# Kernel tuning notes

Measured on AMD Instinct MI355X. Metric: run time of the kernel, lower is better.

## Reference

```python
import jax, jax.numpy as jnp
import numpy as np

BN_EPS = 1e-5
HIDDEN = 64
NUM_LAYERS = 8


def setup_inputs() -> dict:
    key = jax.random.key(0)
    ks = jax.random.split(key, 24)
    N, E, G = 100000, 1600000, 500
    H, L = HIDDEN, NUM_LAYERS
    rn = lambda k, s, sc=0.1: jax.random.normal(k, s, jnp.float32) * sc
    un = lambda k, s: jax.random.uniform(k, s, jnp.float32, 0.5, 1.5)
    inp = {}
    inp["x"] = jax.random.normal(ks[0], (N, 1), jnp.float32)
    inp["edge_index"] = jax.random.randint(ks[1], (2, E), 0, N, jnp.int32)
    inp["batch"] = jnp.sort(jax.random.randint(ks[2], (N,), 0, G, jnp.int32))
    inp["num_graphs"] = G
    inp["eps"] = rn(ks[3], (L,))
    inp["W1_first"] = rn(ks[4], (1, H))
    inp["W1_rest"] = rn(ks[5], (L - 1, H, H))
    inp["b1"] = rn(ks[6], (L, H))
    inp["g1"] = un(ks[7], (L, H))
    inp["be1"] = rn(ks[8], (L, H))
    inp["m1"] = rn(ks[9], (L, H))
    inp["v1"] = un(ks[10], (L, H))
    inp["W2"] = rn(ks[11], (L, H, H))
    inp["b2"] = rn(ks[12], (L, H))
    inp["g2"] = un(ks[13], (L, H))
    inp["be2"] = rn(ks[14], (L, H))
    inp["m2"] = rn(ks[15], (L, H))
    inp["v2"] = un(ks[16], (L, H))
    inp["lin1_w"] = rn(ks[17], (L * H, H), 0.05)
    inp["lin1_b"] = rn(ks[18], (H,))
    inp["lin2_w"] = rn(ks[19], (H, 3))
    inp["lin2_b"] = rn(ks[20], (3,))
    return inp


def _bn(h, g, b, m, v):
    # BatchNorm1d in eval mode: affine normalize with running stats
    return (h - m) * jax.lax.rsqrt(v + BN_EPS) * g + b


def reference(x, edge_index, batch, num_graphs, eps, W1_first, W1_rest, b1, g1,
              be1, m1, v1, W2, b2, g2, be2, m2, v2, lin1_w, lin1_b, lin2_w, lin2_b):
    src, dst = edge_index[0], edge_index[1]
    N = x.shape[0]
    h = x
    xs = []
    for i in range(NUM_LAYERS):
        # GINConv: scatter-add neighbor aggregation + (1+eps)*self, then MLP
        agg = jax.ops.segment_sum(h[src], dst, num_segments=N)  # [N, H_in]
        z = (1.0 + eps[i]) * h + agg
        W1 = W1_first if i == 0 else W1_rest[i - 1]
        z = jnp.maximum(z @ W1 + b1[i], 0.0)
        z = _bn(z, g1[i], be1[i], m1[i], v1[i])
        z = jnp.maximum(z @ W2[i] + b2[i], 0.0)
        z = _bn(z, g2[i], be2[i], m2[i], v2[i])
        h = z
        xs.append(h)
    jk = jnp.concatenate(xs, axis=-1)  # [N, L*H] JumpingKnowledge 'cat'
    sums = jax.ops.segment_sum(jk, batch, num_segments=num_graphs)
    counts = jax.ops.segment_sum(jnp.ones((N,), jk.dtype), batch, num_segments=num_graphs)
    pooled = sums / jnp.maximum(counts, 1.0)[:, None]  # global_mean_pool
    h = jnp.maximum(pooled @ lin1_w + lin1_b, 0.0)
    # dropout is identity in eval mode
    logits = h @ lin2_w + lin2_b
    return jax.nn.log_softmax(logits, axis=-1)
```

## Files before the change

kernel.cpp:

```cpp
#include <hip/hip_runtime.h>
#include <hip/hip_bf16.h>
#include <math.h>


typedef unsigned int uint;
typedef unsigned short ushort;
typedef __attribute__((ext_vector_type(8))) short short8;
typedef __attribute__((ext_vector_type(4))) float floatx4;
typedef __attribute__((ext_vector_type(4))) uint uintx4;

#define BBITS 10
#define BCAP 20480
#define BMASK ((1 << BBITS) - 1)

__device__ __forceinline__ float bf_lo(uint w) { return __uint_as_float(w << 16); }
__device__ __forceinline__ float bf_hi(uint w) { return __uint_as_float(w & 0xffff0000u); }

__device__ __forceinline__ ushort f2bf(float x) {
  __hip_bfloat16 h = __float2bfloat16(x);
  return *(ushort*)&h;
}
__device__ __forceinline__ float bf2f(ushort u) { return __uint_as_float((uint)u << 16); }

__device__ __forceinline__ uint pack_bf16(float a, float b) {
  return (uint)f2bf(a) | ((uint)f2bf(b) << 16);
}

__device__ __forceinline__ float slot_combine(float v) {
  return v + __shfl_xor(v, 8, 64);
}

__device__ __forceinline__ void split8(float4 u0, float4 u1, short8& hi, short8& lo) {
  float v0 = u0.x, v1 = u0.y, v2 = u0.z, v3 = u0.w;
  float v4 = u1.x, v5 = u1.y, v6 = u1.z, v7 = u1.w;
  ushort h0 = f2bf(v0), h1 = f2bf(v1), h2 = f2bf(v2), h3 = f2bf(v3);
  ushort h4 = f2bf(v4), h5 = f2bf(v5), h6 = f2bf(v6), h7 = f2bf(v7);
  hi[0] = (short)h0; hi[1] = (short)h1; hi[2] = (short)h2; hi[3] = (short)h3;
  hi[4] = (short)h4; hi[5] = (short)h5; hi[6] = (short)h6; hi[7] = (short)h7;
  lo[0] = (short)f2bf(v0 - bf2f(h0)); lo[1] = (short)f2bf(v1 - bf2f(h1));
  lo[2] = (short)f2bf(v2 - bf2f(h2)); lo[3] = (short)f2bf(v3 - bf2f(h3));
  lo[4] = (short)f2bf(v4 - bf2f(h4)); lo[5] = (short)f2bf(v5 - bf2f(h5));
  lo[6] = (short)f2bf(v6 - bf2f(h6)); lo[7] = (short)f2bf(v7 - bf2f(h7));
}


__global__ void init_bc_kernel(int* __restrict__ bc, int NB) {
  int b = threadIdx.x;
  if (b < NB) bc[b * 16] = b * BCAP;
}

__global__ __launch_bounds__(1024) void bin_edges_kernel(
    const int* __restrict__ src, const int* __restrict__ dst, int* __restrict__ bc,
    uint* __restrict__ arena, int E) {
  __shared__ int cnt[128], base[128];
  for (long chunk = (long)blockIdx.x * 4096; chunk < E; chunk += (long)gridDim.x * 4096) {
    if (threadIdx.x < 128) cnt[threadIdx.x] = 0;
    __syncthreads();
    uint v[4];
    int b[4], r[4];
#pragma unroll
    for (int u = 0; u < 4; ++u) {
      long e = chunk + threadIdx.x + u * 1024;
      if (e < E) {
        int s = src[e];
        int d = dst[e];
        b[u] = d >> BBITS;
        v[u] = ((uint)s << BBITS) | (uint)(d & BMASK);
        r[u] = atomicAdd(&cnt[b[u]], 1);
      }
    }
    __syncthreads();
    if (threadIdx.x < 128)
      base[threadIdx.x] = cnt[threadIdx.x] ? atomicAdd(&bc[threadIdx.x * 16], cnt[threadIdx.x]) : 0;
    __syncthreads();
#pragma unroll
    for (int u = 0; u < 4; ++u) {
      long e = chunk + threadIdx.x + u * 1024;
      if (e < E) arena[base[b[u]] + r[u]] = v[u];
    }
    __syncthreads();
  }
}

__global__ __launch_bounds__(1024) void bucket_count_kernel(
    const uint* __restrict__ arena, const int* __restrict__ bc,
    int* __restrict__ deg, int N) {
  __shared__ int hist[1 << BBITS];
  int b = blockIdx.x;
  int lo = b << BBITS;
  int hi = min(lo + (1 << BBITS), N);
  hist[threadIdx.x] = 0;
  __syncthreads();
  int cnt = bc[b * 16] - b * BCAP;
  const uint* ad = arena + (size_t)b * BCAP;
  for (int i = threadIdx.x; i < cnt; i += 1024) atomicAdd(&hist[ad[i] & BMASK], 1);
  __syncthreads();
  if (lo + (int)threadIdx.x < hi) deg[lo + threadIdx.x] = hist[threadIdx.x];
}

__global__ __launch_bounds__(1024) void bucket_scatter_kernel(
    const uint* __restrict__ arena, const int* __restrict__ bc,
    const int* __restrict__ rp, int* __restrict__ col, int N) {
  __shared__ int cur[1 << BBITS];
  int b = blockIdx.x;
  int lo = b << BBITS;
  int hi = min(lo + (1 << BBITS), N);
  if (lo + (int)threadIdx.x < hi) cur[threadIdx.x] = rp[lo + threadIdx.x];
  __syncthreads();
  int cnt = bc[b * 16] - b * BCAP;
  const uint* ad = arena + (size_t)b * BCAP;
  for (int i = threadIdx.x; i < cnt; i += 1024) {
    uint v = ad[i];
    int pos = atomicAdd(&cur[v & BMASK], 1);
    col[pos] = (int)(v >> BBITS);
  }
}

__global__ void scan_blocksums(const int* __restrict__ deg, int* __restrict__ bsum, int N) {
  __shared__ int red[256];
  int i = blockIdx.x * 256 + threadIdx.x;
  red[threadIdx.x] = (i < N) ? deg[i] : 0;
  __syncthreads();
  for (int off = 128; off > 0; off >>= 1) {
    if (threadIdx.x < off) red[threadIdx.x] += red[threadIdx.x + off];
    __syncthreads();
  }
  if (threadIdx.x == 0) bsum[blockIdx.x] = red[0];
}

__global__ void scan_bsum(const int* __restrict__ bsum, int* __restrict__ boff,
                          int* __restrict__ rp_last, int B) {
  __shared__ int tmp[1024];
  int t = threadIdx.x;
  int v = (t < B) ? bsum[t] : 0;
  tmp[t] = v;
  __syncthreads();
  for (int off = 1; off < 1024; off <<= 1) {
    int u = (t >= off) ? tmp[t - off] : 0;
    __syncthreads();
    tmp[t] += u;
    __syncthreads();
  }
  if (t < B) boff[t] = tmp[t] - v;
  if (t == 1023) *rp_last = tmp[1023];
}

__global__ void scan_final(const int* __restrict__ deg, const int* __restrict__ boff,
                           int* __restrict__ rp, int N) {
  __shared__ int tmp[256];
  int i = blockIdx.x * 256 + threadIdx.x;
  int v = (i < N) ? deg[i] : 0;
  tmp[threadIdx.x] = v;
  __syncthreads();
  for (int off = 1; off < 256; off <<= 1) {
    int u = (threadIdx.x >= off) ? tmp[threadIdx.x - off] : 0;
    __syncthreads();
    tmp[threadIdx.x] += u;
    __syncthreads();
  }
  if (i < N) rp[i] = boff[blockIdx.x] + tmp[threadIdx.x] - v;
}

__global__ void graph_bounds_kernel(const int* __restrict__ batch, int* __restrict__ gs,
                                    int N, int G) {
  int n = blockIdx.x * 256 + threadIdx.x;
  if (n >= N) return;
  int b = batch[n];
  int bp = (n == 0) ? -1 : batch[n - 1];
  for (int g = bp + 1; g <= b; ++g) gs[g] = n;
  if (n == N - 1)
    for (int g = b + 1; g <= G; ++g) gs[g] = N;
}

__global__ void prepack_w_kernel(const float* __restrict__ W1_rest,
                                 const float* __restrict__ W2, ushort* __restrict__ wp) {
  int l = blockIdx.x >> 1, g = blockIdx.x & 1;
  const float* W;
  if (g == 0) {
    if (l == 0) return;
    W = W1_rest + (size_t)(l - 1) * 4096;
  } else {
    W = W2 + (size_t)l * 4096;
  }
  ushort* out = wp + (size_t)(l * 2 + g) * 8192;
  for (int idx = threadIdx.x; idx < 4096; idx += blockDim.x) {
    int j = idx & 7, lane = (idx >> 3) & 63, ks = (idx >> 9) & 1, nt = (idx >> 10) & 3;
    int k = ks * 32 + (lane >> 4) * 8 + j;
    int n = nt * 16 + (lane & 15);
    float w = W[k * 64 + n];
    ushort hi = f2bf(w);
    ushort lo = f2bf(w - bf2f(hi));
    size_t base = (size_t)((nt * 2 + ks) * 2) * 512 + lane * 8 + j;
    out[base] = hi;
    out[base + 512] = lo;
  }
}

__global__ __launch_bounds__(256, 8) void agg_kernel(
    const ushort* __restrict__ hb, const int* __restrict__ rp,
    const int* __restrict__ col, const float* __restrict__ eps,
    int layer, ushort* __restrict__ zb, int N) {
  int lane = threadIdx.x & 63;
  int ni = lane >> 4;
  int s = (lane >> 3) & 1;
  int r = lane & 7;
  int wave = blockIdx.x * (blockDim.x >> 6) + (threadIdx.x >> 6);
  int nwaves = gridDim.x * (blockDim.x >> 6);
  float ep = 1.0f + eps[layer];
  for (int qb = wave * 4; qb < N; qb += nwaves * 4) {
    int node = qb + ni;
    bool valid = node < N;
    int nn = valid ? node : (N - 1);
    int beg = rp[nn];
    int end = valid ? rp[nn + 1] : beg;
    float a[8] = {0.f, 0.f, 0.f, 0.f, 0.f, 0.f, 0.f, 0.f};
    int e = beg + s;
    while (e < end) {
      int e1 = (e + 2 < end) ? (e + 2) : e;
      int e2 = (e + 4 < end) ? (e + 4) : e;
      int e3 = (e + 6 < end) ? (e + 6) : e;
      float m1 = (e + 2 < end) ? 1.0f : 0.0f;
      float m2 = (e + 4 < end) ? 1.0f : 0.0f;
      float m3 = (e + 6 < end) ? 1.0f : 0.0f;
      int c0 = __builtin_nontemporal_load(col + e);
      int c1 = __builtin_nontemporal_load(col + e1);
      int c2 = __builtin_nontemporal_load(col + e2);
      int c3 = __builtin_nontemporal_load(col + e3);
      uint4 w0 = ((const uint4*)(hb + (long)c0 * 64))[r];
      uint4 w1 = ((const uint4*)(hb + (long)c1 * 64))[r];
      uint4 w2 = ((const uint4*)(hb + (long)c2 * 64))[r];
      uint4 w3 = ((const uint4*)(hb + (long)c3 * 64))[r];
      a[0] += bf_lo(w0.x); a[1] += bf_hi(w0.x);
      a[2] += bf_lo(w0.y); a[3] += bf_hi(w0.y);
      a[4] += bf_lo(w0.z); a[5] += bf_hi(w0.z);
      a[6] += bf_lo(w0.w); a[7] += bf_hi(w0.w);
      a[0] = fmaf(m1, bf_lo(w1.x), a[0]); a[1] = fmaf(m1, bf_hi(w1.x), a[1]);
      a[2] = fmaf(m1, bf_lo(w1.y), a[2]); a[3] = fmaf(m1, bf_hi(w1.y), a[3]);
      a[4] = fmaf(m1, bf_lo(w1.z), a[4]); a[5] = fmaf(m1, bf_hi(w1.z), a[5]);
      a[6] = fmaf(m1, bf_lo(w1.w), a[6]); a[7] = fmaf(m1, bf_hi(w1.w), a[7]);
      a[0] = fmaf(m2, bf_lo(w2.x), a[0]); a[1] = fmaf(m2, bf_hi(w2.x), a[1]);
      a[2] = fmaf(m2, bf_lo(w2.y), a[2]); a[3] = fmaf(m2, bf_hi(w2.y), a[3]);
      a[4] = fmaf(m2, bf_lo(w2.z), a[4]); a[5] = fmaf(m2, bf_hi(w2.z), a[5]);
      a[6] = fmaf(m2, bf_lo(w2.w), a[6]); a[7] = fmaf(m2, bf_hi(w2.w), a[7]);
      a[0] = fmaf(m3, bf_lo(w3.x), a[0]); a[1] = fmaf(m3, bf_hi(w3.x), a[1]);
      a[2] = fmaf(m3, bf_lo(w3.y), a[2]); a[3] = fmaf(m3, bf_hi(w3.y), a[3]);
      a[4] = fmaf(m3, bf_lo(w3.z), a[4]); a[5] = fmaf(m3, bf_hi(w3.z), a[5]);
      a[6] = fmaf(m3, bf_lo(w3.w), a[6]); a[7] = fmaf(m3, bf_hi(w3.w), a[7]);
      e += 8;
    }
#pragma unroll
    for (int j = 0; j < 8; ++j) a[j] = slot_combine(a[j]);
    if (s == 0 && valid) {
      uint4 hv = ((const uint4*)(hb + (long)node * 64))[r];
      float v0 = fmaf(ep, bf_lo(hv.x), a[0]), v1 = fmaf(ep, bf_hi(hv.x), a[1]);
      float v2 = fmaf(ep, bf_lo(hv.y), a[2]), v3 = fmaf(ep, bf_hi(hv.y), a[3]);
      float v4 = fmaf(ep, bf_lo(hv.z), a[4]), v5 = fmaf(ep, bf_hi(hv.z), a[5]);
      float v6 = fmaf(ep, bf_lo(hv.w), a[6]), v7 = fmaf(ep, bf_hi(hv.w), a[7]);
      uintx4 w;
      w.x = pack_bf16(v0, v1); w.y = pack_bf16(v2, v3);
      w.z = pack_bf16(v4, v5); w.w = pack_bf16(v6, v7);
      __builtin_nontemporal_store(w, (uintx4*)(zb + (size_t)node * 64 + r * 8));
    }
  }
}

__global__ __launch_bounds__(512) void mfma_mlp_kernel(
    const ushort* __restrict__ zb, const float* __restrict__ z0,
    const float* __restrict__ W1f, ushort* __restrict__ hout,
    const ushort* __restrict__ wp1, const ushort* __restrict__ wp2,
    const float* __restrict__ b1, const float* __restrict__ g1,
    const float* __restrict__ be1, const float* __restrict__ m1,
    const float* __restrict__ v1,
    const float* __restrict__ b2, const float* __restrict__ g2,
    const float* __restrict__ be2, const float* __restrict__ m2,
    const float* __restrict__ v2,
    const int* __restrict__ batch, float* __restrict__ pooled,
    int layer, int skip1, int N) {
  __shared__ float bnp[6][64];
  __shared__ float w1fl[64];
  __shared__ float sbuf[128][68];
  __shared__ int batchl[128];
  int tid = threadIdx.x;
  int blockbase = blockIdx.x * 128;
  if (tid < 64) {
    bnp[0][tid] = b1[tid];
    float s1 = g1[tid] * rsqrtf(v1[tid] + 1e-5f);
    bnp[1][tid] = s1;
    bnp[2][tid] = be1[tid] - m1[tid] * s1;
    bnp[3][tid] = b2[tid];
    float s2 = g2[tid] * rsqrtf(v2[tid] + 1e-5f);
    bnp[4][tid] = s2;
    bnp[5][tid] = be2[tid] - m2[tid] * s2;
    if (skip1) w1fl[tid] = W1f[tid];
  }
  if (tid < 128) batchl[tid] = (blockbase + tid < N) ? batch[blockbase + tid] : -1;
  __syncthreads();
  int wave = tid >> 6, lane = tid & 63;
  int q = lane >> 4, c = lane & 15;
  int base = blockbase + wave * 16;
  int srow = wave * 16;

  short8 ahi0, alo0, ahi1, alo1;
  if (!skip1) {
    {
      long row = base + c;
      if (row >= N) row = N - 1;
      const ushort* zr = zb + row * 64;
      ahi0 = __builtin_nontemporal_load((const short8*)(zr + q * 8));
      ahi1 = __builtin_nontemporal_load((const short8*)(zr + 32 + q * 8));
    }
    floatx4 acc[4];
#pragma unroll
    for (int nt = 0; nt < 4; ++nt) acc[nt] = (floatx4){0.f, 0.f, 0.f, 0.f};
#pragma unroll
    for (int nt = 0; nt < 4; ++nt) {
#pragma unroll
      for (int ks = 0; ks < 2; ++ks) {
        const ushort* fb = wp1 + ((nt * 2 + ks) * 2) * 512 + lane * 8;
        short8 bh = *(const short8*)fb;
        short8 bl = *(const short8*)(fb + 512);
        short8 ah = ks ? ahi1 : ahi0;
        acc[nt] = __builtin_amdgcn_mfma_f32_16x16x32_bf16(ah, bh, acc[nt], 0, 0, 0);
        acc[nt] = __builtin_amdgcn_mfma_f32_16x16x32_bf16(ah, bl, acc[nt], 0, 0, 0);
      }
    }
#pragma unroll
    for (int nt = 0; nt < 4; ++nt) {
      int feat = nt * 16 + c;
      float s1 = bnp[1][feat], o1 = bnp[2][feat], bb = bnp[0][feat];
#pragma unroll
      for (int r = 0; r < 4; ++r) {
        float y = fmaxf(acc[nt][r] + bb, 0.f);
        sbuf[srow + q * 4 + r][feat] = fmaf(y, s1, o1);
      }
    }
    float4 u0 = *(const float4*)&sbuf[srow + c][q * 8];
    float4 u1 = *(const float4*)&sbuf[srow + c][q * 8 + 4];
    split8(u0, u1, ahi0, alo0);
    u0 = *(const float4*)&sbuf[srow + c][32 + q * 8];
    u1 = *(const float4*)&sbuf[srow + c][32 + q * 8 + 4];
    split8(u0, u1, ahi1, alo1);
  } else {
    long row = base + c;
    if (row >= N) row = N - 1;
    float zv = z0[row];
    float4 t00, t01, t10, t11;
    {
      float tv[8];
#pragma unroll
      for (int j = 0; j < 8; ++j) {
        int k = q * 8 + j;
        float y = fmaxf(fmaf(zv, w1fl[k], bnp[0][k]), 0.f);
        tv[j] = fmaf(y, bnp[1][k], bnp[2][k]);
      }
      t00 = make_float4(tv[0], tv[1], tv[2], tv[3]);
      t01 = make_float4(tv[4], tv[5], tv[6], tv[7]);
#pragma unroll
      for (int j = 0; j < 8; ++j) {
        int k = 32 + q * 8 + j;
        float y = fmaxf(fmaf(zv, w1fl[k], bnp[0][k]), 0.f);
        tv[j] = fmaf(y, bnp[1][k], bnp[2][k]);
      }
      t10 = make_float4(tv[0], tv[1], tv[2], tv[3]);
      t11 = make_float4(tv[4], tv[5], tv[6], tv[7]);
    }
    split8(t00, t01, ahi0, alo0);
    split8(t10, t11, ahi1, alo1);
  }

  floatx4 acc2[4];
#pragma unroll
  for (int nt = 0; nt < 4; ++nt) acc2[nt] = (floatx4){0.f, 0.f, 0.f, 0.f};
#pragma unroll
  for (int nt = 0; nt < 4; ++nt) {
#pragma unroll
    for (int ks = 0; ks < 2; ++ks) {
      const ushort* fb = wp2 + ((nt * 2 + ks) * 2) * 512 + lane * 8;
      short8 bh = *(const short8*)fb;
      short8 bl = *(const short8*)(fb + 512);
      short8 ah = ks ? ahi1 : ahi0;
      short8 al = ks ? alo1 : alo0;
      acc2[nt] = __builtin_amdgcn_mfma_f32_16x16x32_bf16(ah, bh, acc2[nt], 0, 0, 0);
      acc2[nt] = __builtin_amdgcn_mfma_f32_16x16x32_bf16(al, bh, acc2[nt], 0, 0, 0);
      acc2[nt] = __builtin_amdgcn_mfma_f32_16x16x32_bf16(ah, bl, acc2[nt], 0, 0, 0);
    }
  }

#pragma unroll
  for (int nt = 0; nt < 4; ++nt) {
    int feat = nt * 16 + c;
    float s2 = bnp[4][feat], o2 = bnp[5][feat], bb = bnp[3][feat];
#pragma unroll
    for (int r = 0; r < 4; ++r) {
      int node = base + q * 4 + r;
      float val = 0.f;
      if (node < N) {
        float y = fmaxf(acc2[nt][r] + bb, 0.f);
        val = fmaf(y, s2, o2);
      }
      sbuf[srow + q * 4 + r][feat] = val;
    }
  }
  __syncthreads();

#pragma unroll
  for (int it = 0; it < 2; ++it) {
    int chunk = tid + it * 512;
    int row = chunk >> 3, c8 = chunk & 7;
    int node = blockbase + row;
    if (node < N) {
      const float* sp = &sbuf[row][c8 * 8];
      uintx4 w;
      w.x = pack_bf16(sp[0], sp[1]);
      w.y = pack_bf16(sp[2], sp[3]);
      w.z = pack_bf16(sp[4], sp[5]);
      w.w = pack_bf16(sp[6], sp[7]);
      *(uintx4*)(hout + (long)node * 64 + c8 * 8) = w;
    }
  }

  if (tid < 256) {
    int j = tid & 63;
    int quarter = tid >> 6;
    int nvalid = N - blockbase;
    if (nvalid > 128) nvalid = 128;
    int i = quarter * 32;
    int iend = i + 32;
    if (iend > nvalid) iend = nvalid;
    while (i < iend) {
      int g = batchl[i];
      float s = 0.f;
      while (i < iend && batchl[i] == g) { s += sbuf[i][j]; ++i; }
      atomicAdd(&pooled[(size_t)g * 512 + layer * 64 + j], s);
    }
  }
}

__global__ void z0_kernel(const float* __restrict__ x, const int* __restrict__ rp,
                          const int* __restrict__ col, const float* __restrict__ eps,
                          float* __restrict__ z0, int N) {
  int n = blockIdx.x * blockDim.x + threadIdx.x;
  if (n >= N) return;
  int beg = rp[n], end = rp[n + 1];
  float a = 0.f;
  for (int e = beg; e < end; ++e) a += x[col[e]];
  z0[n] = fmaf(1.0f + eps[0], x[n], a);
}

__global__ __launch_bounds__(64) void final_kernel(
    const float* __restrict__ pooled, const int* __restrict__ gs,
    const float* __restrict__ lin1_w, const float* __restrict__ lin1_b,
    const float* __restrict__ lin2_w, const float* __restrict__ lin2_b,
    float* __restrict__ out, int G) {
  int g = blockIdx.x;
  int j = threadIdx.x;
  float inv = 1.0f / fmaxf((float)(gs[g + 1] - gs[g]), 1.0f);
  __shared__ float p[512];
  for (int t = j; t < 512; t += 64) p[t] = pooled[(long)g * 512 + t] * inv;
  __syncthreads();
  float a0 = lin1_b[j], a1 = 0.f, a2 = 0.f, a3 = 0.f;
  for (int k = 0; k < 512; k += 4) {
    a0 = fmaf(p[k + 0], lin1_w[(k + 0) * 64 + j], a0);
    a1 = fmaf(p[k + 1], lin1_w[(k + 1) * 64 + j], a1);
    a2 = fmaf(p[k + 2], lin1_w[(k + 2) * 64 + j], a2);
    a3 = fmaf(p[k + 3], lin1_w[(k + 3) * 64 + j], a3);
  }
  float hv = fmaxf((a0 + a1) + (a2 + a3), 0.f);
  __shared__ float hb[64];
  hb[j] = hv;
  __syncthreads();
  __shared__ float lg[3];
  if (j < 3) {
    float a = lin2_b[j];
#pragma unroll
    for (int k = 0; k < 64; ++k) a = fmaf(hb[k], lin2_w[k * 3 + j], a);
    lg[j] = a;
  }
  __syncthreads();
  if (j < 3) {
    float mx = fmaxf(fmaxf(lg[0], lg[1]), lg[2]);
    float lse = mx + logf(expf(lg[0] - mx) + expf(lg[1] - mx) + expf(lg[2] - mx));
    out[g * 3 + j] = lg[j] - lse;
  }
}

extern "C" void kernel_launch(void* const* d_in, const int* in_sizes, int n_in,
                              void* d_out, int out_size, void* d_ws, size_t ws_size,
                              hipStream_t stream) {
  const float* x        = (const float*)d_in[0];
  const int*   edge     = (const int*)d_in[1];
  const int*   batch    = (const int*)d_in[2];
  const float* eps      = (const float*)d_in[4];
  const float* W1_first = (const float*)d_in[5];
  const float* W1_rest  = (const float*)d_in[6];
  const float* b1       = (const float*)d_in[7];
  const float* g1       = (const float*)d_in[8];
  const float* be1      = (const float*)d_in[9];
  const float* m1       = (const float*)d_in[10];
  const float* v1       = (const float*)d_in[11];
  const float* W2       = (const float*)d_in[12];
  const float* b2       = (const float*)d_in[13];
  const float* g2       = (const float*)d_in[14];
  const float* be2      = (const float*)d_in[15];
  const float* m2       = (const float*)d_in[16];
  const float* v2       = (const float*)d_in[17];
  const float* lin1_w   = (const float*)d_in[18];
  const float* lin1_b   = (const float*)d_in[19];
  const float* lin2_w   = (const float*)d_in[20];
  const float* lin2_b   = (const float*)d_in[21];

  int N = in_sizes[0];
  int E = in_sizes[1] / 2;
  int G = out_size / 3;
  const int* esrc = edge;
  const int* edst = edge + E;
  int NB = (N + (1 << BBITS) - 1) >> BBITS;
  if (NB > 128) NB = 128;

  size_t off = 0;
  auto alloc = [&](size_t bytes) -> char* {
    char* p = (char*)d_ws + off;
    off += (bytes + 255) & ~(size_t)255;
    return p;
  };
  int SB = (N + 255) / 256;
  int*    deg    = (int*)alloc((size_t)N * 4);
  int*    rp     = (int*)alloc((size_t)(N + 1) * 4);
  int*    col    = (int*)alloc((size_t)E * 4);
  int*    bsum   = (int*)alloc((size_t)SB * 4);
  int*    boff   = (int*)alloc((size_t)SB * 4);
  int*    bc     = (int*)alloc((size_t)128 * 16 * 4);
  uint*   arena  = (uint*)alloc((size_t)NB * BCAP * 4);
  int*    gs     = (int*)alloc((size_t)(G + 1) * 4);
  ushort* wpack  = (ushort*)alloc((size_t)16 * 8192 * 2);
  float*  z0buf  = (float*)alloc((size_t)N * 4);
  ushort* zbuf   = (ushort*)alloc((size_t)N * 64 * 2);
  ushort* hA     = (ushort*)alloc((size_t)N * 64 * 2);
  ushort* hB     = (ushort*)alloc((size_t)N * 64 * 2);
  float*  pooled = (float*)alloc((size_t)G * 512 * 4);
  (void)ws_size;

  init_bc_kernel<<<1, 128, 0, stream>>>(bc, NB);
  int ebA = (E + 4095) / 4096;
  bin_edges_kernel<<<ebA, 1024, 0, stream>>>(esrc, edst, bc, arena, E);
  bucket_count_kernel<<<NB, 1024, 0, stream>>>(arena, bc, deg, N);
  scan_blocksums<<<SB, 256, 0, stream>>>(deg, bsum, N);
  scan_bsum<<<1, 1024, 0, stream>>>(bsum, boff, rp + N, SB);
  scan_final<<<SB, 256, 0, stream>>>(deg, boff, rp, N);
  bucket_scatter_kernel<<<NB, 1024, 0, stream>>>(arena, bc, rp, col, N);

  graph_bounds_kernel<<<SB, 256, 0, stream>>>(batch, gs, N, G);
  prepack_w_kernel<<<16, 256, 0, stream>>>(W1_rest, W2, wpack);
  (void)hipMemsetAsync(pooled, 0, (size_t)G * 512 * 4, stream);

  int nb = (N + 127) / 128;
  z0_kernel<<<SB, 256, 0, stream>>>(x, rp, col, eps, z0buf, N);
  mfma_mlp_kernel<<<nb, 512, 0, stream>>>(zbuf, z0buf, W1_first, hA,
      wpack, wpack + 8192,
      b1, g1, be1, m1, v1, b2, g2, be2, m2, v2, batch, pooled, 0, 1, N);

  ushort* hin = hA;
  ushort* hout = hB;
  for (int i = 1; i < 8; ++i) {
    agg_kernel<<<2048, 256, 0, stream>>>(hin, rp, col, eps, i, zbuf, N);
    mfma_mlp_kernel<<<nb, 512, 0, stream>>>(zbuf, z0buf, W1_first, hout,
        wpack + (size_t)(2 * i) * 8192, wpack + (size_t)(2 * i + 1) * 8192,
        b1 + i * 64, g1 + i * 64, be1 + i * 64, m1 + i * 64, v1 + i * 64,
        b2 + i * 64, g2 + i * 64, be2 + i * 64, m2 + i * 64, v2 + i * 64,
        batch, pooled, i, 0, N);
    ushort* t = hin; hin = hout; hout = t;
  }
  final_kernel<<<G, 64, 0, stream>>>(pooled, gs, lin1_w, lin1_b,
                                     lin2_w, lin2_b, (float*)d_out, G);
}
```

Baseline: 573.0 us.

## Fuse neighbor aggregation into the per-layer MFMA MLP kernel

Removes the separate agg_kernel and performs the CSR gather-sum inside the MLP kernel, with each wave aggregating its 16 rows into shared memory before the MFMA. This eliminates the zbuf round trip through global memory and one kernel launch per layer. In exchange the gather now runs in 512-thread blocks with whatever occupancy the MLP kernel gets, possibly hiding gather latency less well than the dedicated 2048-block grid, and the A operand now uses only the hi bf16 part of the fp32 sum.

```diff
diff --git a/kernel.cpp b/kernel.cpp
--- a/kernel.cpp
+++ b/kernel.cpp
@@ -43,6 +43,15 @@
   lo[6] = (short)f2bf(v6 - bf2f(h6)); lo[7] = (short)f2bf(v7 - bf2f(h7));
 }
 
+__device__ __forceinline__ short8 hi8(float4 u0, float4 u1) {
+  short8 h;
+  h[0] = (short)f2bf(u0.x); h[1] = (short)f2bf(u0.y);
+  h[2] = (short)f2bf(u0.z); h[3] = (short)f2bf(u0.w);
+  h[4] = (short)f2bf(u1.x); h[5] = (short)f2bf(u1.y);
+  h[6] = (short)f2bf(u1.z); h[7] = (short)f2bf(u1.w);
+  return h;
+}
+
 
 __global__ void init_bc_kernel(int* __restrict__ bc, int NB) {
   int b = threadIdx.x;
@@ -196,77 +205,11 @@
   }
 }
 
-__global__ __launch_bounds__(256, 8) void agg_kernel(
-    const ushort* __restrict__ hb, const int* __restrict__ rp,
-    const int* __restrict__ col, const float* __restrict__ eps,
-    int layer, ushort* __restrict__ zb, int N) {
-  int lane = threadIdx.x & 63;
-  int ni = lane >> 4;
-  int s = (lane >> 3) & 1;
-  int r = lane & 7;
-  int wave = blockIdx.x * (blockDim.x >> 6) + (threadIdx.x >> 6);
-  int nwaves = gridDim.x * (blockDim.x >> 6);
-  float ep = 1.0f + eps[layer];
-  for (int qb = wave * 4; qb < N; qb += nwaves * 4) {
-    int node = qb + ni;
-    bool valid = node < N;
-    int nn = valid ? node : (N - 1);
-    int beg = rp[nn];
-    int end = valid ? rp[nn + 1] : beg;
-    float a[8] = {0.f, 0.f, 0.f, 0.f, 0.f, 0.f, 0.f, 0.f};
-    int e = beg + s;
-    while (e < end) {
-      int e1 = (e + 2 < end) ? (e + 2) : e;
-      int e2 = (e + 4 < end) ? (e + 4) : e;
-      int e3 = (e + 6 < end) ? (e + 6) : e;
-      float m1 = (e + 2 < end) ? 1.0f : 0.0f;
-      float m2 = (e + 4 < end) ? 1.0f : 0.0f;
-      float m3 = (e + 6 < end) ? 1.0f : 0.0f;
-      int c0 = __builtin_nontemporal_load(col + e);
-      int c1 = __builtin_nontemporal_load(col + e1);
-      int c2 = __builtin_nontemporal_load(col + e2);
-      int c3 = __builtin_nontemporal_load(col + e3);
-      uint4 w0 = ((const uint4*)(hb + (long)c0 * 64))[r];
-      uint4 w1 = ((const uint4*)(hb + (long)c1 * 64))[r];
-      uint4 w2 = ((const uint4*)(hb + (long)c2 * 64))[r];
-      uint4 w3 = ((const uint4*)(hb + (long)c3 * 64))[r];
-      a[0] += bf_lo(w0.x); a[1] += bf_hi(w0.x);
-      a[2] += bf_lo(w0.y); a[3] += bf_hi(w0.y);
-      a[4] += bf_lo(w0.z); a[5] += bf_hi(w0.z);
-      a[6] += bf_lo(w0.w); a[7] += bf_hi(w0.w);
-      a[0] = fmaf(m1, bf_lo(w1.x), a[0]); a[1] = fmaf(m1, bf_hi(w1.x), a[1]);
-      a[2] = fmaf(m1, bf_lo(w1.y), a[2]); a[3] = fmaf(m1, bf_hi(w1.y), a[3]);
-      a[4] = fmaf(m1, bf_lo(w1.z), a[4]); a[5] = fmaf(m1, bf_hi(w1.z), a[5]);
-      a[6] = fmaf(m1, bf_lo(w1.w), a[6]); a[7] = fmaf(m1, bf_hi(w1.w), a[7]);
-      a[0] = fmaf(m2, bf_lo(w2.x), a[0]); a[1] = fmaf(m2, bf_hi(w2.x), a[1]);
-      a[2] = fmaf(m2, bf_lo(w2.y), a[2]); a[3] = fmaf(m2, bf_hi(w2.y), a[3]);
-      a[4] = fmaf(m2, bf_lo(w2.z), a[4]); a[5] = fmaf(m2, bf_hi(w2.z), a[5]);
-      a[6] = fmaf(m2, bf_lo(w2.w), a[6]); a[7] = fmaf(m2, bf_hi(w2.w), a[7]);
-      a[0] = fmaf(m3, bf_lo(w3.x), a[0]); a[1] = fmaf(m3, bf_hi(w3.x), a[1]);
-      a[2] = fmaf(m3, bf_lo(w3.y), a[2]); a[3] = fmaf(m3, bf_hi(w3.y), a[3]);
-      a[4] = fmaf(m3, bf_lo(w3.z), a[4]); a[5] = fmaf(m3, bf_hi(w3.z), a[5]);
-      a[6] = fmaf(m3, bf_lo(w3.w), a[6]); a[7] = fmaf(m3, bf_hi(w3.w), a[7]);
-      e += 8;
-    }
-#pragma unroll
-    for (int j = 0; j < 8; ++j) a[j] = slot_combine(a[j]);
-    if (s == 0 && valid) {
-      uint4 hv = ((const uint4*)(hb + (long)node * 64))[r];
-      float v0 = fmaf(ep, bf_lo(hv.x), a[0]), v1 = fmaf(ep, bf_hi(hv.x), a[1]);
-      float v2 = fmaf(ep, bf_lo(hv.y), a[2]), v3 = fmaf(ep, bf_hi(hv.y), a[3]);
-      float v4 = fmaf(ep, bf_lo(hv.z), a[4]), v5 = fmaf(ep, bf_hi(hv.z), a[5]);
-      float v6 = fmaf(ep, bf_lo(hv.w), a[6]), v7 = fmaf(ep, bf_hi(hv.w), a[7]);
-      uintx4 w;
-      w.x = pack_bf16(v0, v1); w.y = pack_bf16(v2, v3);
-      w.z = pack_bf16(v4, v5); w.w = pack_bf16(v6, v7);
-      __builtin_nontemporal_store(w, (uintx4*)(zb + (size_t)node * 64 + r * 8));
-    }
-  }
-}
-
-__global__ __launch_bounds__(512) void mfma_mlp_kernel(
-    const ushort* __restrict__ zb, const float* __restrict__ z0,
+__global__ __launch_bounds__(512) void fused_layer_kernel(
+    const ushort* __restrict__ hb, const float* __restrict__ z0,
     const float* __restrict__ W1f, ushort* __restrict__ hout,
+    const int* __restrict__ rp, const int* __restrict__ col,
+    const float* __restrict__ eps,
     const ushort* __restrict__ wp1, const ushort* __restrict__ wp2,
     const float* __restrict__ b1, const float* __restrict__ g1,
     const float* __restrict__ be1, const float* __restrict__ m1,
@@ -302,12 +245,71 @@
 
   short8 ahi0, alo0, ahi1, alo1;
   if (!skip1) {
+    int ni = lane >> 4;
+    int s = (lane >> 3) & 1;
+    int r = lane & 7;
+    float ep = 1.0f + eps[layer];
+    for (int qq = 0; qq < 4; ++qq) {
+      int node = base + qq * 4 + ni;
+      bool valid = node < N;
+      int nn = valid ? node : (N - 1);
+      int beg = rp[nn];
+      int end = valid ? rp[nn + 1] : beg;
+      float a[8] = {0.f, 0.f, 0.f, 0.f, 0.f, 0.f, 0.f, 0.f};
+      int e = beg + s;
+      while (e < end) {
+        int e1 = (e + 2 < end) ? (e + 2) : e;
+        int e2 = (e + 4 < end) ? (e + 4) : e;
+        int e3 = (e + 6 < end) ? (e + 6) : e;
+        float m1v = (e + 2 < end) ? 1.0f : 0.0f;
+        float m2v = (e + 4 < end) ? 1.0f : 0.0f;
+        float m3v = (e + 6 < end) ? 1.0f : 0.0f;
+        int c0 = __builtin_nontemporal_load(col + e);
+        int c1 = __builtin_nontemporal_load(col + e1);
+        int c2 = __builtin_nontemporal_load(col + e2);
+        int c3 = __builtin_nontemporal_load(col + e3);
+        uint4 w0 = ((const uint4*)(hb + (long)c0 * 64))[r];
+        uint4 w1 = ((const uint4*)(hb + (long)c1 * 64))[r];
+        uint4 w2 = ((const uint4*)(hb + (long)c2 * 64))[r];
+        uint4 w3 = ((const uint4*)(hb + (long)c3 * 64))[r];
+        a[0] += bf_lo(w0.x); a[1] += bf_hi(w0.x);
+        a[2] += bf_lo(w0.y); a[3] += bf_hi(w0.y);
+        a[4] += bf_lo(w0.z); a[5] += bf_hi(w0.z);
+        a[6] += bf_lo(w0.w); a[7] += bf_hi(w0.w);
+        a[0] = fmaf(m1v, bf_lo(w1.x), a[0]); a[1] = fmaf(m1v, bf_hi(w1.x), a[1]);
+        a[2] = fmaf(m1v, bf_lo(w1.y), a[2]); a[3] = fmaf(m1v, bf_hi(w1.y), a[3]);
+        a[4] = fmaf(m1v, bf_lo(w1.z), a[4]); a[5] = fmaf(m1v, bf_hi(w1.z), a[5]);
+        a[6] = fmaf(m1v, bf_lo(w1.w), a[6]); a[7] = fmaf(m1v, bf_hi(w1.w), a[7]);
+        a[0] = fmaf(m2v, bf_lo(w2.x), a[0]); a[1] = fmaf(m2v, bf_hi(w2.x), a[1]);
+        a[2] = fmaf(m2v, bf_lo(w2.y), a[2]); a[3] = fmaf(m2v, bf_hi(w2.y), a[3]);
+        a[4] = fmaf(m2v, bf_lo(w2.z), a[4]); a[5] = fmaf(m2v, bf_hi(w2.z), a[5]);
+        a[6] = fmaf(m2v, bf_lo(w2.w), a[6]); a[7] = fmaf(m2v, bf_hi(w2.w), a[7]);
+        a[0] = fmaf(m3v, bf_lo(w3.x), a[0]); a[1] = fmaf(m3v, bf_hi(w3.x), a[1]);
+        a[2] = fmaf(m3v, bf_lo(w3.y), a[2]); a[3] = fmaf(m3v, bf_hi(w3.y), a[3]);
+        a[4] = fmaf(m3v, bf_lo(w3.z), a[4]); a[5] = fmaf(m3v, bf_hi(w3.z), a[5]);
+        a[6] = fmaf(m3v, bf_lo(w3.w), a[6]); a[7] = fmaf(m3v, bf_hi(w3.w), a[7]);
+        e += 8;
+      }
+#pragma unroll
+      for (int j = 0; j < 8; ++j) a[j] = slot_combine(a[j]);
+      if (s == 0) {
+        uint4 hv = ((const uint4*)(hb + (long)nn * 64))[r];
+        float v0 = fmaf(ep, bf_lo(hv.x), a[0]), v1 = fmaf(ep, bf_hi(hv.x), a[1]);
+        float v2 = fmaf(ep, bf_lo(hv.y), a[2]), v3 = fmaf(ep, bf_hi(hv.y), a[3]);
+        float v4 = fmaf(ep, bf_lo(hv.z), a[4]), v5 = fmaf(ep, bf_hi(hv.z), a[5]);
+        float v6 = fmaf(ep, bf_lo(hv.w), a[6]), v7 = fmaf(ep, bf_hi(hv.w), a[7]);
+        int row = srow + qq * 4 + ni;
+        *(float4*)&sbuf[row][r * 8] = make_float4(v0, v1, v2, v3);
+        *(float4*)&sbuf[row][r * 8 + 4] = make_float4(v4, v5, v6, v7);
+      }
+    }
     {
-      long row = base + c;
-      if (row >= N) row = N - 1;
-      const ushort* zr = zb + row * 64;
-      ahi0 = __builtin_nontemporal_load((const short8*)(zr + q * 8));
-      ahi1 = __builtin_nontemporal_load((const short8*)(zr + 32 + q * 8));
+      float4 u0 = *(const float4*)&sbuf[srow + c][q * 8];
+      float4 u1 = *(const float4*)&sbuf[srow + c][q * 8 + 4];
+      ahi0 = hi8(u0, u1);
+      u0 = *(const float4*)&sbuf[srow + c][32 + q * 8];
+      u1 = *(const float4*)&sbuf[srow + c][32 + q * 8 + 4];
+      ahi1 = hi8(u0, u1);
     }
     floatx4 acc[4];
 #pragma unroll
@@ -329,9 +331,9 @@
       int feat = nt * 16 + c;
       float s1 = bnp[1][feat], o1 = bnp[2][feat], bb = bnp[0][feat];
 #pragma unroll
-      for (int r = 0; r < 4; ++r) {
-        float y = fmaxf(acc[nt][r] + bb, 0.f);
-        sbuf[srow + q * 4 + r][feat] = fmaf(y, s1, o1);
+      for (int r2 = 0; r2 < 4; ++r2) {
+        float y = fmaxf(acc[nt][r2] + bb, 0.f);
+        sbuf[srow + q * 4 + r2][feat] = fmaf(y, s1, o1);
       }
     }
     float4 u0 = *(const float4*)&sbuf[srow + c][q * 8];
@@ -391,14 +393,14 @@
     int feat = nt * 16 + c;
     float s2 = bnp[4][feat], o2 = bnp[5][feat], bb = bnp[3][feat];
 #pragma unroll
-    for (int r = 0; r < 4; ++r) {
-      int node = base + q * 4 + r;
+    for (int r2 = 0; r2 < 4; ++r2) {
+      int node = base + q * 4 + r2;
       float val = 0.f;
       if (node < N) {
-        float y = fmaxf(acc2[nt][r] + bb, 0.f);
+        float y = fmaxf(acc2[nt][r2] + bb, 0.f);
         val = fmaf(y, s2, o2);
       }
-      sbuf[srow + q * 4 + r][feat] = val;
+      sbuf[srow + q * 4 + r2][feat] = val;
     }
   }
   __syncthreads();
@@ -534,7 +536,6 @@
   int*    gs     = (int*)alloc((size_t)(G + 1) * 4);
   ushort* wpack  = (ushort*)alloc((size_t)16 * 8192 * 2);
   float*  z0buf  = (float*)alloc((size_t)N * 4);
-  ushort* zbuf   = (ushort*)alloc((size_t)N * 64 * 2);
   ushort* hA     = (ushort*)alloc((size_t)N * 64 * 2);
   ushort* hB     = (ushort*)alloc((size_t)N * 64 * 2);
   float*  pooled = (float*)alloc((size_t)G * 512 * 4);
@@ -555,15 +556,15 @@
 
   int nb = (N + 127) / 128;
   z0_kernel<<<SB, 256, 0, stream>>>(x, rp, col, eps, z0buf, N);
-  mfma_mlp_kernel<<<nb, 512, 0, stream>>>(zbuf, z0buf, W1_first, hA,
-      wpack, wpack + 8192,
+  fused_layer_kernel<<<nb, 512, 0, stream>>>(hA, z0buf, W1_first, hA,
+      rp, col, eps, wpack, wpack + 8192,
       b1, g1, be1, m1, v1, b2, g2, be2, m2, v2, batch, pooled, 0, 1, N);
 
   ushort* hin = hA;
   ushort* hout = hB;
   for (int i = 1; i < 8; ++i) {
-    agg_kernel<<<2048, 256, 0, stream>>>(hin, rp, col, eps, i, zbuf, N);
-    mfma_mlp_kernel<<<nb, 512, 0, stream>>>(zbuf, z0buf, W1_first, hout,
+    fused_layer_kernel<<<nb, 512, 0, stream>>>(hin, z0buf, W1_first, hout,
+        rp, col, eps,
         wpack + (size_t)(2 * i) * 8192, wpack + (size_t)(2 * i + 1) * 8192,
         b1 + i * 64, g1 + i * 64, be1 + i * 64, m1 + i * 64, v1 + i * 64,
         b2 + i * 64, g2 + i * 64, be2 + i * 64, m2 + i * 64, v2 + i * 64,
```

Result: faster. 517.6 us (median of 2 runs) (-9.7%).
